# Performance work log

Hardware: AMD Instinct MI355X
Metric: run time of the kernel (lower is better)

Reference implementation:

```python
import jax, jax.numpy as jnp
import numpy as np

P = 2.0
EPS = 1e-06

def _dist(x1, x2):
    # torch.dist(x1, x2, p=2): p-norm of flattened difference per sample -> [B]
    d = x1 - x2
    return jnp.sqrt(jnp.sum(d * d, axis=-1))

def setup_inputs() -> dict:
    key = jax.random.key(0)
    k1, k2, k3 = jax.random.split(key, 3)
    B, D = 65536, 256
    return {
        "anchor": jax.random.normal(k1, (B, D), dtype=jnp.float32),
        "positive": jax.random.normal(k2, (B, D), dtype=jnp.float32),
        "negative": jax.random.normal(k3, (B, D), dtype=jnp.float32),
    }

def reference(anchor, positive, negative):
    d_ap = _dist(anchor, positive)          # [B]
    d_an = _dist(anchor, negative)          # [B]
    d_pn = _dist(positive, negative)        # [B]
    margin_sim = 1.0 + 2.0 / (jnp.exp(4.0 * d_ap) + EPS)
    margin_dissim = 1.0 + 2.0 / (jnp.exp(-(4.0 * d_an) + 4.0) + EPS)
    margin = margin_sim + margin_dissim
    loss = d_ap - (d_an + d_pn) / 2.0 + margin
    return jnp.mean(loss)  # reduction='mean'
```

## Files before the change

### kernel.cpp

```cpp
#include <hip/hip_runtime.h>
#include <math.h>


#define D 256
#define TPB 256
#define ROWS_PER_WAVE 8
#define WAVES_PER_BLOCK 4
#define ROWS_PER_BLOCK 32

typedef float nt_float4 __attribute__((ext_vector_type(4)));

__global__ __launch_bounds__(TPB, 3) void triplet_partial(
    const nt_float4* __restrict__ a4, const nt_float4* __restrict__ p4,
    const nt_float4* __restrict__ n4, float* __restrict__ partial, int B)
{
    const int lane = threadIdx.x & 63;
    const int wib  = threadIdx.x >> 6;
    const int row0 = (blockIdx.x * WAVES_PER_BLOCK + wib) * ROWS_PER_WAVE;

    float sap[ROWS_PER_WAVE], san[ROWS_PER_WAVE], spn[ROWS_PER_WAVE];

    if (row0 + ROWS_PER_WAVE <= B) {
        const size_t base = (size_t)row0 * 64 + lane;

        nt_float4 av[ROWS_PER_WAVE], pv[ROWS_PER_WAVE], nv[ROWS_PER_WAVE];
        #pragma unroll
        for (int j = 0; j < ROWS_PER_WAVE; ++j)
            av[j] = __builtin_nontemporal_load(a4 + base + (size_t)j * 64);
        #pragma unroll
        for (int j = 0; j < ROWS_PER_WAVE; ++j)
            pv[j] = __builtin_nontemporal_load(p4 + base + (size_t)j * 64);
        #pragma unroll
        for (int j = 0; j < ROWS_PER_WAVE; ++j)
            nv[j] = __builtin_nontemporal_load(n4 + base + (size_t)j * 64);

        #pragma unroll
        for (int j = 0; j < ROWS_PER_WAVE; ++j) {
            float d, s0, s1, s2;
            d = av[j].x - pv[j].x; s0 = d * d;
            d = av[j].y - pv[j].y; s0 = fmaf(d, d, s0);
            d = av[j].z - pv[j].z; s0 = fmaf(d, d, s0);
            d = av[j].w - pv[j].w; s0 = fmaf(d, d, s0);
            d = av[j].x - nv[j].x; s1 = d * d;
            d = av[j].y - nv[j].y; s1 = fmaf(d, d, s1);
            d = av[j].z - nv[j].z; s1 = fmaf(d, d, s1);
            d = av[j].w - nv[j].w; s1 = fmaf(d, d, s1);
            d = pv[j].x - nv[j].x; s2 = d * d;
            d = pv[j].y - nv[j].y; s2 = fmaf(d, d, s2);
            d = pv[j].z - nv[j].z; s2 = fmaf(d, d, s2);
            d = pv[j].w - nv[j].w; s2 = fmaf(d, d, s2);
            sap[j] = s0; san[j] = s1; spn[j] = s2;
        }
    } else {
        #pragma unroll
        for (int j = 0; j < ROWS_PER_WAVE; ++j) {
            sap[j] = 0.0f; san[j] = 0.0f; spn[j] = 0.0f;
        }
    }

    #pragma unroll
    for (int off = 32; off >= 1; off >>= 1) {
        #pragma unroll
        for (int j = 0; j < ROWS_PER_WAVE; ++j) {
            sap[j] += __shfl_xor(sap[j], off, 64);
            san[j] += __shfl_xor(san[j], off, 64);
            spn[j] += __shfl_xor(spn[j], off, 64);
        }
    }

    __shared__ float sm[WAVES_PER_BLOCK];
    if (lane == 0) {
        float local = 0.0f;
        if (row0 + ROWS_PER_WAVE <= B) {
            #pragma unroll
            for (int j = 0; j < ROWS_PER_WAVE; ++j) {
                const float dap = sqrtf(sap[j]);
                const float dan = sqrtf(san[j]);
                const float dpn = sqrtf(spn[j]);
                const float msim = 1.0f + 2.0f / (__expf(4.0f * dap) + 1e-6f);
                const float mdis = 1.0f + 2.0f / (__expf(-4.0f * dan + 4.0f) + 1e-6f);
                local += dap - 0.5f * (dan + dpn) + msim + mdis;
            }
        }
        sm[wib] = local;
    }
    __syncthreads();
    if (threadIdx.x == 0) {
        float s = 0.0f;
        #pragma unroll
        for (int i = 0; i < WAVES_PER_BLOCK; ++i) s += sm[i];
        partial[blockIdx.x] = s;
    }
}

__global__ __launch_bounds__(256) void final_reduce(
    const float* __restrict__ partial, float* __restrict__ out,
    int nPartial, float invB)
{
    float s = 0.0f;
    for (int i = threadIdx.x; i < nPartial; i += blockDim.x) s += partial[i];
    #pragma unroll
    for (int off = 32; off > 0; off >>= 1) s += __shfl_xor(s, off, 64);

    __shared__ float sm[4];
    const int lane = threadIdx.x & 63;
    const int w = threadIdx.x >> 6;
    if (lane == 0) sm[w] = s;
    __syncthreads();
    if (threadIdx.x == 0) out[0] = (sm[0] + sm[1] + sm[2] + sm[3]) * invB;
}

extern "C" void kernel_launch(void* const* d_in, const int* in_sizes, int n_in,
                              void* d_out, int out_size, void* d_ws, size_t ws_size,
                              hipStream_t stream) {
    const nt_float4* a = (const nt_float4*)d_in[0];
    const nt_float4* p = (const nt_float4*)d_in[1];
    const nt_float4* n = (const nt_float4*)d_in[2];
    float* out = (float*)d_out;
    float* partial = (float*)d_ws;

    const int B = in_sizes[0] / D;
    const int nBlocks = (B + ROWS_PER_BLOCK - 1) / ROWS_PER_BLOCK;

    triplet_partial<<<nBlocks, TPB, 0, stream>>>(a, p, n, partial, B);
    final_reduce<<<1, 256, 0, stream>>>(partial, out, nBlocks, 1.0f / (float)B);
}
```

Baseline: 179.4 us.

## Use transposing pack-merge shuffle reduction and double rows per wave

Raises rows per wave from 8 to 16 and replaces the per-row butterfly shuffle reduction with a recursive-halving pack-merge. Each shuffle stage now halves the number of live partial sums, so the 16 rows finish spread across lane groups and every lane computes the per-row epilogue in parallel, where before lane 0 did it serially. The epilogue results are scaled by 0.25 to account for each row being replicated across four lanes, then reduced across the wave. Doubling the rows per wave also doubles the in-flight loads per thread and raises register pressure, while launch bounds now request 4 blocks instead of 3.

```diff
diff --git a/kernel.cpp b/kernel.cpp
--- a/kernel.cpp
+++ b/kernel.cpp
@@ -4,24 +4,32 @@
 
 #define D 256
 #define TPB 256
-#define ROWS_PER_WAVE 8
+#define ROWS_PER_WAVE 16
 #define WAVES_PER_BLOCK 4
-#define ROWS_PER_BLOCK 32
+#define ROWS_PER_BLOCK (ROWS_PER_WAVE * WAVES_PER_BLOCK)
 
 typedef float nt_float4 __attribute__((ext_vector_type(4)));
 
-__global__ __launch_bounds__(TPB, 3) void triplet_partial(
+__device__ __forceinline__ float pack_merge(float lo, float hi, int mask, int lane) {
+    const bool up = (lane & mask) != 0;
+    const float send = up ? lo : hi;
+    const float recv = __shfl_xor(send, mask, 64);
+    return (up ? hi : lo) + recv;
+}
+
+__global__ __launch_bounds__(TPB, 4) void triplet_partial(
     const nt_float4* __restrict__ a4, const nt_float4* __restrict__ p4,
     const nt_float4* __restrict__ n4, float* __restrict__ partial, int B)
 {
     const int lane = threadIdx.x & 63;
     const int wib  = threadIdx.x >> 6;
-    const int row0 = (blockIdx.x * WAVES_PER_BLOCK + wib) * ROWS_PER_WAVE;
+    const int g    = blockIdx.x * WAVES_PER_BLOCK + wib;
+    const bool inRange = (g + 1) * ROWS_PER_WAVE <= B;
 
     float sap[ROWS_PER_WAVE], san[ROWS_PER_WAVE], spn[ROWS_PER_WAVE];
 
-    if (row0 + ROWS_PER_WAVE <= B) {
-        const size_t base = (size_t)row0 * 64 + lane;
+    if (inRange) {
+        const size_t base = (size_t)g * (ROWS_PER_WAVE * 64) + lane;
 
         nt_float4 av[ROWS_PER_WAVE], pv[ROWS_PER_WAVE], nv[ROWS_PER_WAVE];
         #pragma unroll
@@ -58,32 +66,50 @@
         }
     }
 
+    float a1[8], n1[8], p1[8];
     #pragma unroll
-    for (int off = 32; off >= 1; off >>= 1) {
-        #pragma unroll
-        for (int j = 0; j < ROWS_PER_WAVE; ++j) {
-            sap[j] += __shfl_xor(sap[j], off, 64);
-            san[j] += __shfl_xor(san[j], off, 64);
-            spn[j] += __shfl_xor(spn[j], off, 64);
-        }
+    for (int r = 0; r < 8; ++r) {
+        a1[r] = pack_merge(sap[2*r], sap[2*r+1], 32, lane);
+        n1[r] = pack_merge(san[2*r], san[2*r+1], 32, lane);
+        p1[r] = pack_merge(spn[2*r], spn[2*r+1], 32, lane);
+    }
+    float a2[4], n2[4], p2[4];
+    #pragma unroll
+    for (int r = 0; r < 4; ++r) {
+        a2[r] = pack_merge(a1[2*r], a1[2*r+1], 16, lane);
+        n2[r] = pack_merge(n1[2*r], n1[2*r+1], 16, lane);
+        p2[r] = pack_merge(p1[2*r], p1[2*r+1], 16, lane);
+    }
+    float a3[2], n3[2], p3[2];
+    #pragma unroll
+    for (int r = 0; r < 2; ++r) {
+        a3[r] = pack_merge(a2[2*r], a2[2*r+1], 8, lane);
+        n3[r] = pack_merge(n2[2*r], n2[2*r+1], 8, lane);
+        p3[r] = pack_merge(p2[2*r], p2[2*r+1], 8, lane);
+    }
+    float fa = pack_merge(a3[0], a3[1], 4, lane);
+    float fn = pack_merge(n3[0], n3[1], 4, lane);
+    float fp = pack_merge(p3[0], p3[1], 4, lane);
+    fa += __shfl_xor(fa, 2, 64); fa += __shfl_xor(fa, 1, 64);
+    fn += __shfl_xor(fn, 2, 64); fn += __shfl_xor(fn, 1, 64);
+    fp += __shfl_xor(fp, 2, 64); fp += __shfl_xor(fp, 1, 64);
+
+    float local = 0.0f;
+    if (inRange) {
+        const float dap = sqrtf(fa);
+        const float dan = sqrtf(fn);
+        const float dpn = sqrtf(fp);
+        const float msim = 1.0f + 2.0f / (__expf(4.0f * dap) + 1e-6f);
+        const float mdis = 1.0f + 2.0f / (__expf(-4.0f * dan + 4.0f) + 1e-6f);
+        local = 0.25f * (dap - 0.5f * (dan + dpn) + msim + mdis);
     }
 
+    #pragma unroll
+    for (int off = 32; off >= 1; off >>= 1)
+        local += __shfl_xor(local, off, 64);
+
     __shared__ float sm[WAVES_PER_BLOCK];
-    if (lane == 0) {
-        float local = 0.0f;
-        if (row0 + ROWS_PER_WAVE <= B) {
-            #pragma unroll
-            for (int j = 0; j < ROWS_PER_WAVE; ++j) {
-                const float dap = sqrtf(sap[j]);
-                const float dan = sqrtf(san[j]);
-                const float dpn = sqrtf(spn[j]);
-                const float msim = 1.0f + 2.0f / (__expf(4.0f * dap) + 1e-6f);
-                const float mdis = 1.0f + 2.0f / (__expf(-4.0f * dan + 4.0f) + 1e-6f);
-                local += dap - 0.5f * (dan + dpn) + msim + mdis;
-            }
-        }
-        sm[wib] = local;
-    }
+    if (lane == 0) sm[wib] = local;
     __syncthreads();
     if (threadIdx.x == 0) {
         float s = 0.0f;
```

Measured after the change: 217.2 us. +21.1%, slower.
